# Kernel tuning notes

Measured on AMD Instinct MI355X. Metric: run time of the kernel, lower is better.

Reference implementation:

```python
import jax, jax.numpy as jnp
import numpy as np

N, L, D = 16, 128, 128
H, C = 8, 16
EPS = 1e-5


def setup_inputs() -> dict:
    key = jax.random.key(0)
    ks = jax.random.split(key, 10)
    s = 0.02
    return {
        "z": jax.random.normal(ks[0], (N, L, L, D), dtype=jnp.float32),
        "ln_w": jnp.ones((D,), jnp.float32),
        "ln_b": jnp.zeros((D,), jnp.float32),
        "Wq": jax.random.normal(ks[1], (D, H * C), jnp.float32) * s,
        "Wk": jax.random.normal(ks[2], (D, H * C), jnp.float32) * s,
        "Wv": jax.random.normal(ks[3], (D, H * C), jnp.float32) * s,
        "Wg": jax.random.normal(ks[4], (D, H * C), jnp.float32) * s,
        "bg": jnp.zeros((H * C,), jnp.float32),
        "Wo": jax.random.normal(ks[5], (H * C, D), jnp.float32) * s,
        "bo": jnp.zeros((D,), jnp.float32),
    }


def reference(z, ln_w, ln_b, Wq, Wk, Wv, Wg, bg, Wo, bo):
    n, l, _, d = z.shape
    # LayerNorm over channel dim
    mu = jnp.mean(z, axis=-1, keepdims=True)
    var = jnp.var(z, axis=-1, keepdims=True)
    zn = (z - mu) * jax.lax.rsqrt(var + EPS) * ln_w + ln_b
    # projections -> (N, L, L, H, C)
    q = (zn @ Wq).reshape(n, l, l, H, C)
    k = (zn @ Wk).reshape(n, l, l, H, C)
    v = (zn @ Wv).reshape(n, l, l, H, C)
    g = jax.nn.sigmoid(zn @ Wg + bg).reshape(n, l, l, H, C)
    # attention over the sample axis N, per pair position (a,b) and head h
    att = jnp.einsum('iabhc,jabhc->ijabh', q, k) * (1.0 / np.sqrt(C))
    att = jax.nn.softmax(att, axis=1)
    o = jnp.einsum('ijabh,jabhc->iabhc', att, v) * g
    out = o.reshape(n, l, l, H * C) @ Wo + bo
    return out
```

## Files before the change

### kernel.cpp

```cpp
#include <hip/hip_runtime.h>
#include <hip/hip_bf16.h>


typedef short bf16x8 __attribute__((ext_vector_type(8)));
typedef float f32x4 __attribute__((ext_vector_type(4)));

#define MFMA16x32(A, B, C) __builtin_amdgcn_mfma_f32_16x16x32_bf16((A), (B), (C), 0, 0, 0)

__device__ __forceinline__ unsigned short f2bf(float f) {
    unsigned int u = __float_as_uint(f);
    u += 0x7fffu + ((u >> 16) & 1u);
    return (unsigned short)(u >> 16);
}

static constexpr int  DD     = 128;
static constexpr int  NPOS   = 128 * 128;
static constexpr long ZSTR   = (long)NPOS * DD;
static constexpr int  ZN_STR = 136;
static constexpr int  SB_STR = 56;
static constexpr int  OB_STR = 132;

__launch_bounds__(256, 2)
__global__ void ssattn_fused(const float* __restrict__ z,
                             const float* __restrict__ ln_w,
                             const float* __restrict__ ln_b,
                             const float* __restrict__ Wq,
                             const float* __restrict__ Wk,
                             const float* __restrict__ Wv,
                             const float* __restrict__ Wg,
                             const float* __restrict__ bg,
                             const float* __restrict__ Wo,
                             const float* __restrict__ bo,
                             float* __restrict__ out)
{
    __shared__ __align__(16) unsigned short zn_s[16 * ZN_STR];
    __shared__ __align__(16) unsigned short ob_s[16 * ZN_STR];
    __shared__ __align__(16) float outb_s[16 * OB_STR];
    __shared__ __align__(16) unsigned short qb_s[4][16 * SB_STR];
    __shared__ __align__(16) unsigned short kq_s[4][16 * SB_STR];
    __shared__ __align__(16) unsigned short vb_s[4][16 * SB_STR];
    __shared__ float lnw_s[DD];
    __shared__ float lnb_s[DD];

    const int tid  = threadIdx.x;
    const int wid  = tid >> 6;
    const int lane = tid & 63;
    const int quad = lane >> 4;
    const int lm   = lane & 15;
    const int r16  = tid >> 4;
    const int s16  = tid & 15;

    if (tid < DD) { lnw_s[tid] = ln_w[tid]; lnb_s[tid] = ln_b[tid]; }
    for (int i = tid; i < 16 * SB_STR; i += 256) {
        qb_s[0][i] = 0; qb_s[1][i] = 0; qb_s[2][i] = 0; qb_s[3][i] = 0;
        kq_s[0][i] = 0; kq_s[1][i] = 0; kq_s[2][i] = 0; kq_s[3][i] = 0;
        vb_s[0][i] = 0; vb_s[1][i] = 0; vb_s[2][i] = 0; vb_s[3][i] = 0;
    }

    bf16x8 wq_r[2][4], wk_r[2][4], wv_r[2][4], wg_r[2][4], wo_r[2][4];
    float bg_r[2], bo_r[2];
#pragma unroll
    for (int hl = 0; hl < 2; ++hl) {
        const int col = (wid * 2 + hl) * 16 + lm;
        bg_r[hl] = bg[col];
        bo_r[hl] = bo[col];
#pragma unroll
        for (int kb = 0; kb < 4; ++kb) {
            const int kbase = kb * 32 + quad * 8;
            bf16x8 a, b, c, d, e;
#pragma unroll
            for (int j = 0; j < 8; ++j) {
                const int k = kbase + j;
                a[j] = (short)f2bf(Wq[k * DD + col]);
                b[j] = (short)f2bf(Wk[k * DD + col]);
                c[j] = (short)f2bf(Wv[k * DD + col]);
                d[j] = (short)f2bf(Wg[k * DD + col]);
                e[j] = (short)f2bf(Wo[k * DD + col]);
            }
            wq_r[hl][kb] = a; wk_r[hl][kb] = b; wv_r[hl][kb] = c;
            wg_r[hl][kb] = d; wo_r[hl][kb] = e;
        }
    }
    __syncthreads();

    unsigned short* const qb = qb_s[wid];
    unsigned short* const kq = kq_s[wid];
    unsigned short* const vb = vb_s[wid];

    for (int p = blockIdx.x; p < NPOS; p += gridDim.x) {
        {
            const float* zp = z + (long)r16 * ZSTR + (long)p * DD + s16 * 8;
            const float4 ra = *(const float4*)zp;
            const float4 rb = *(const float4*)(zp + 4);
            float x[8] = {ra.x, ra.y, ra.z, ra.w, rb.x, rb.y, rb.z, rb.w};
            float s = 0.f, ss = 0.f;
#pragma unroll
            for (int j = 0; j < 8; ++j) { s += x[j]; ss += x[j] * x[j]; }
#pragma unroll
            for (int m = 1; m <= 8; m <<= 1) {
                s  += __shfl_xor(s,  m, 16);
                ss += __shfl_xor(ss, m, 16);
            }
            const float mu = s * (1.f / 128.f);
            const float rs = rsqrtf(ss * (1.f / 128.f) - mu * mu + 1e-5f);
            unsigned int pk[4];
#pragma unroll
            for (int jj = 0; jj < 4; ++jj) {
                const int c0 = s16 * 8 + jj * 2;
                const unsigned short lo = f2bf((x[jj * 2]     - mu) * rs * lnw_s[c0]     + lnb_s[c0]);
                const unsigned short hi = f2bf((x[jj * 2 + 1] - mu) * rs * lnw_s[c0 + 1] + lnb_s[c0 + 1]);
                pk[jj] = (unsigned)lo | ((unsigned)hi << 16);
            }
            uint4 st; st.x = pk[0]; st.y = pk[1]; st.z = pk[2]; st.w = pk[3];
            *(uint4*)&zn_s[r16 * ZN_STR + s16 * 8] = st;
        }
        __syncthreads();

        bf16x8 af[4];
#pragma unroll
        for (int kb = 0; kb < 4; ++kb)
            af[kb] = *(const bf16x8*)&zn_s[lm * ZN_STR + kb * 32 + quad * 8];

#pragma unroll
        for (int hl = 0; hl < 2; ++hl) {
            f32x4 aq = {0,0,0,0}, ak = {0,0,0,0}, av = {0,0,0,0}, ag = {0,0,0,0};
#pragma unroll
            for (int kb = 0; kb < 4; ++kb) {
                aq = MFMA16x32(af[kb], wq_r[hl][kb], aq);
                ak = MFMA16x32(af[kb], wk_r[hl][kb], ak);
                av = MFMA16x32(af[kb], wv_r[hl][kb], av);
                ag = MFMA16x32(af[kb], wg_r[hl][kb], ag);
            }
#pragma unroll
            for (int r = 0; r < 4; ++r) {
                const int row = quad * 4 + r;
                qb[row * SB_STR + lm] = f2bf(aq[r] * 0.25f);
                kq[row * SB_STR + lm] = f2bf(ak[r]);
                vb[lm * SB_STR + row] = f2bf(av[r]);
            }
            float gv[4];
#pragma unroll
            for (int r = 0; r < 4; ++r)
                gv[r] = 1.f / (1.f + __expf(-(ag[r] + bg_r[hl])));

            const bf16x8 aqf = *(const bf16x8*)&qb[lm * SB_STR + quad * 8];
            const bf16x8 bkf = *(const bf16x8*)&kq[lm * SB_STR + quad * 8];
            const f32x4 z4 = {0,0,0,0};
            f32x4 att = MFMA16x32(aqf, bkf, z4);

            f32x4 pr;
#pragma unroll
            for (int r = 0; r < 4; ++r) {
                const float a = att[r];
                float mx = a;
#pragma unroll
                for (int m = 1; m <= 8; m <<= 1) mx = fmaxf(mx, __shfl_xor(mx, m, 16));
                const float ex = __expf(a - mx);
                float sm = ex;
#pragma unroll
                for (int m = 1; m <= 8; m <<= 1) sm += __shfl_xor(sm, m, 16);
                pr[r] = ex / sm;
            }
#pragma unroll
            for (int r = 0; r < 4; ++r)
                qb[(quad * 4 + r) * SB_STR + lm] = f2bf(pr[r]);

            const bf16x8 apf = *(const bf16x8*)&qb[lm * SB_STR + quad * 8];
            const bf16x8 bvf = *(const bf16x8*)&vb[lm * SB_STR + quad * 8];
            f32x4 oc = MFMA16x32(apf, bvf, z4);

            const int hcol = (wid * 2 + hl) * 16 + lm;
#pragma unroll
            for (int r = 0; r < 4; ++r)
                ob_s[(quad * 4 + r) * ZN_STR + hcol] = f2bf(oc[r] * gv[r]);
        }
        __syncthreads();

        bf16x8 of[4];
#pragma unroll
        for (int kb = 0; kb < 4; ++kb)
            of[kb] = *(const bf16x8*)&ob_s[lm * ZN_STR + kb * 32 + quad * 8];
#pragma unroll
        for (int hl = 0; hl < 2; ++hl) {
            f32x4 acc = {0,0,0,0};
#pragma unroll
            for (int kb = 0; kb < 4; ++kb)
                acc = MFMA16x32(of[kb], wo_r[hl][kb], acc);
            const int col = (wid * 2 + hl) * 16 + lm;
#pragma unroll
            for (int r = 0; r < 4; ++r)
                outb_s[(quad * 4 + r) * OB_STR + col] = acc[r] + bo_r[hl];
        }
        __syncthreads();

        {
            float* op = out + (long)r16 * ZSTR + (long)p * DD + s16 * 8;
            const float* sp = &outb_s[r16 * OB_STR + s16 * 8];
            float4 v0 = *(const float4*)(sp);
            float4 v1 = *(const float4*)(sp + 4);
            *(float4*)(op)     = v0;
            *(float4*)(op + 4) = v1;
        }
        __syncthreads();
    }
}

extern "C" void kernel_launch(void* const* d_in, const int* in_sizes, int n_in,
                              void* d_out, int out_size, void* d_ws, size_t ws_size,
                              hipStream_t stream) {
    (void)in_sizes; (void)n_in; (void)out_size; (void)d_ws; (void)ws_size;
    ssattn_fused<<<dim3(512), dim3(256), 0, stream>>>(
        (const float*)d_in[0],
        (const float*)d_in[1],
        (const float*)d_in[2],
        (const float*)d_in[3],
        (const float*)d_in[4],
        (const float*)d_in[5],
        (const float*)d_in[6],
        (const float*)d_in[7],
        (const float*)d_in[8],
        (const float*)d_in[9],
        (float*)d_out);
}
```

Before: 342.7 us.

## Prefetch next z tile, store output directly, double grid and occupancy

Loads the next position's z values into registers before the output projection, so the global read latency overlaps with compute. Drops the shared-memory output staging buffer and its two barriers, writing projection results straight to global memory with narrower per-lane stores. Launches 1024 blocks with a fixed iteration count and raises the launch-bounds occupancy target to 4, which may force register spills given the large set of register-resident weight fragments. It also adds a redundant Wg load line that has no effect on results.

New measurement: 511.1 us. +49.2%, slower.

```diff
diff --git a/kernel.cpp b/kernel.cpp
--- a/kernel.cpp
+++ b/kernel.cpp
@@ -18,9 +18,10 @@
 static constexpr long ZSTR   = (long)NPOS * DD;
 static constexpr int  ZN_STR = 136;
 static constexpr int  SB_STR = 56;
-static constexpr int  OB_STR = 132;
-
-__launch_bounds__(256, 2)
+static constexpr int  NBLK   = 1024;
+static constexpr int  ITERS  = NPOS / NBLK;
+
+__launch_bounds__(256, 4)
 __global__ void ssattn_fused(const float* __restrict__ z,
                              const float* __restrict__ ln_w,
                              const float* __restrict__ ln_b,
@@ -35,7 +36,6 @@
 {
     __shared__ __align__(16) unsigned short zn_s[16 * ZN_STR];
     __shared__ __align__(16) unsigned short ob_s[16 * ZN_STR];
-    __shared__ __align__(16) float outb_s[16 * OB_STR];
     __shared__ __align__(16) unsigned short qb_s[4][16 * SB_STR];
     __shared__ __align__(16) unsigned short kq_s[4][16 * SB_STR];
     __shared__ __align__(16) unsigned short vb_s[4][16 * SB_STR];
@@ -74,9 +74,11 @@
                 a[j] = (short)f2bf(Wq[k * DD + col]);
                 b[j] = (short)f2bf(Wk[k * DD + col]);
                 c[j] = (short)f2bf(Wv[k * DD + col]);
-                d[j] = (short)f2bf(Wg[k * DD + col]);
+                d[j] = (short)f2bf(Wv == Wk ? 0.f : Wg[k * DD + col]);
                 e[j] = (short)f2bf(Wo[k * DD + col]);
             }
+#pragma unroll
+            for (int j = 0; j < 8; ++j) d[j] = (short)f2bf(Wg[(kbase + j) * DD + col]);
             wq_r[hl][kb] = a; wk_r[hl][kb] = b; wv_r[hl][kb] = c;
             wg_r[hl][kb] = d; wo_r[hl][kb] = e;
         }
@@ -87,11 +89,16 @@
     unsigned short* const kq = kq_s[wid];
     unsigned short* const vb = vb_s[wid];
 
-    for (int p = blockIdx.x; p < NPOS; p += gridDim.x) {
+    long pos = blockIdx.x;
+    float4 ra, rb;
+    {
+        const float* zp = z + (long)r16 * ZSTR + pos * DD + s16 * 8;
+        ra = *(const float4*)zp;
+        rb = *(const float4*)(zp + 4);
+    }
+
+    for (int it = 0; it < ITERS; ++it) {
         {
-            const float* zp = z + (long)r16 * ZSTR + (long)p * DD + s16 * 8;
-            const float4 ra = *(const float4*)zp;
-            const float4 rb = *(const float4*)(zp + 4);
             float x[8] = {ra.x, ra.y, ra.z, ra.w, rb.x, rb.y, rb.z, rb.w};
             float s = 0.f, ss = 0.f;
 #pragma unroll
@@ -176,32 +183,31 @@
         }
         __syncthreads();
 
-        bf16x8 of[4];
-#pragma unroll
-        for (int kb = 0; kb < 4; ++kb)
-            of[kb] = *(const bf16x8*)&ob_s[lm * ZN_STR + kb * 32 + quad * 8];
-#pragma unroll
-        for (int hl = 0; hl < 2; ++hl) {
-            f32x4 acc = {0,0,0,0};
+        const long pnext = pos + NBLK;
+        if (it + 1 < ITERS) {
+            const float* zp = z + (long)r16 * ZSTR + pnext * DD + s16 * 8;
+            ra = *(const float4*)zp;
+            rb = *(const float4*)(zp + 4);
+        }
+
+        {
+            bf16x8 of[4];
 #pragma unroll
             for (int kb = 0; kb < 4; ++kb)
-                acc = MFMA16x32(of[kb], wo_r[hl][kb], acc);
-            const int col = (wid * 2 + hl) * 16 + lm;
-#pragma unroll
-            for (int r = 0; r < 4; ++r)
-                outb_s[(quad * 4 + r) * OB_STR + col] = acc[r] + bo_r[hl];
-        }
-        __syncthreads();
-
-        {
-            float* op = out + (long)r16 * ZSTR + (long)p * DD + s16 * 8;
-            const float* sp = &outb_s[r16 * OB_STR + s16 * 8];
-            float4 v0 = *(const float4*)(sp);
-            float4 v1 = *(const float4*)(sp + 4);
-            *(float4*)(op)     = v0;
-            *(float4*)(op + 4) = v1;
-        }
-        __syncthreads();
+                of[kb] = *(const bf16x8*)&ob_s[lm * ZN_STR + kb * 32 + quad * 8];
+#pragma unroll
+            for (int hl = 0; hl < 2; ++hl) {
+                f32x4 acc = {0,0,0,0};
+#pragma unroll
+                for (int kb = 0; kb < 4; ++kb)
+                    acc = MFMA16x32(of[kb], wo_r[hl][kb], acc);
+                const int col = (wid * 2 + hl) * 16 + lm;
+#pragma unroll
+                for (int r = 0; r < 4; ++r)
+                    out[(long)(quad * 4 + r) * ZSTR + pos * DD + col] = acc[r] + bo_r[hl];
+            }
+        }
+        pos = pnext;
     }
 }
 
@@ -209,7 +215,7 @@
                               void* d_out, int out_size, void* d_ws, size_t ws_size,
                               hipStream_t stream) {
     (void)in_sizes; (void)n_in; (void)out_size; (void)d_ws; (void)ws_size;
-    ssattn_fused<<<dim3(512), dim3(256), 0, stream>>>(
+    ssattn_fused<<<dim3(NBLK), dim3(256), 0, stream>>>(
         (const float*)d_in[0],
         (const float*)d_in[1],
         (const float*)d_in[2],
```
